# Performance work log

Hardware: AMD Instinct MI355X
Metric: run time of the kernel (lower is better)

Reference implementation:

```python
import jax, jax.numpy as jnp
import numpy as np

B, R, N, DN, DR, H, Q, NB = 32, 10, 512, 128, 128, 128, 256, 16


def setup_inputs() -> dict:
    key = jax.random.key(0)
    ks = jax.random.split(key, 14)
    inp = {
        'node_features': jax.random.normal(ks[0], (B, N, DN), jnp.float32),
        'relation_features': jax.random.normal(ks[1], (B, R, DR), jnp.float32),
        'adj': jax.random.uniform(ks[2], (B, R, N, N), jnp.float32),
        'obs': jax.random.normal(ks[3], (B, Q, H), jnp.float32),
        'node_mask': jnp.ones((B, N), jnp.float32),
        'obs_mask': jnp.ones((B, Q), jnp.float32),
        # RGCN params (single layer: hidden_dims=[128])
        'Wb': jax.random.normal(ks[4], (NB, (DN + DR) * R), jnp.float32) * 0.02,  # bottleneck (no bias)
        'Ww': jax.random.normal(ks[5], (H, NB), jnp.float32) * 0.1,               # weight (no bias)
        'rgcn_bias': jnp.zeros((), jnp.float32),                                   # scalar bias (filled 0)
        # ContextQueryAttention params
        'w_C': jax.random.normal(ks[6], (H,), jnp.float32) * 0.05,
        'w_Q': jax.random.normal(ks[7], (H,), jnp.float32) * 0.05,
        'w_CQ': jax.random.normal(ks[8], (H,), jnp.float32) * 0.05,
        'cq_bias': jnp.zeros((), jnp.float32),
        # ReprAggregator output linear (shared for both directions)
        'lin_W': jax.random.normal(ks[9], (H, 4 * H), jnp.float32) * 0.02,
        'lin_b': jnp.zeros((H,), jnp.float32),
    }
    return inp


def _masked_softmax(s, mask, axis):
    return jax.nn.softmax(jnp.where(mask > 0, s, -jnp.inf), axis=axis)


def _rgcn(node_features, relation_features, adj, Wb, Ww, rgcn_bias):
    b, n = node_features.shape[0], node_features.shape[1]
    # per-relation concat: (B,R,N,DN+DR)
    nf = jnp.broadcast_to(node_features[:, None], (b, R, n, node_features.shape[-1]))
    rf = jnp.broadcast_to(relation_features[:, :, None, :], (b, R, n, relation_features.shape[-1]))
    cat = jnp.concatenate([nf, rf], axis=-1)
    # per-relation bmm, gathered in relation order along feature dim: (B,N,R*(DN+DR))
    sup = jnp.einsum('brnm,brmd->bnrd', adj, cat)
    sup = sup.reshape(b, n, R * cat.shape[-1])
    h = sup @ Wb.T            # (B,N,NB)
    h = h @ Ww.T              # (B,N,H)
    return jax.nn.sigmoid(h + rgcn_bias)


def _cqattn(ctx, query, ctx_mask, query_mask, w_C, w_Q, w_CQ, cq_bias):
    # trilinear similarity: (B,Lc,Lq)
    res_C = ctx @ w_C                                  # (B,Lc)
    res_Q = query @ w_Q                                # (B,Lq)
    res_CQ = jnp.einsum('bch,bqh->bcq', ctx * w_CQ, query)
    S = res_C[:, :, None] + res_Q[:, None, :] + res_CQ + cq_bias
    s_ctx = _masked_softmax(S, ctx_mask[:, :, None], axis=1)     # softmax over ctx dim
    s_query = _masked_softmax(S, query_mask[:, None, :], axis=2)  # softmax over query dim
    P = jnp.einsum('bcq,bqh->bch', s_query, query)
    Qm = jnp.einsum('bcq,bdq,bdh->bch', s_query, s_ctx, ctx)
    return jnp.concatenate([ctx, P, ctx * P, ctx * Qm], axis=-1)  # (B,Lc,4H)


def reference(node_features, relation_features, adj, obs, node_mask, obs_mask,
              Wb, Ww, rgcn_bias, w_C, w_Q, w_CQ, cq_bias, lin_W, lin_b):
    # GraphEncoder (single RGCN layer)
    node_repr = _rgcn(node_features, relation_features, adj, Wb, Ww, rgcn_bias)
    # ReprAggregator between obs text repr and node repr
    a1 = _cqattn(obs, node_repr, obs_mask, node_mask, w_C, w_Q, w_CQ, cq_bias)
    a2 = _cqattn(node_repr, obs, node_mask, obs_mask, w_C, w_Q, w_CQ, cq_bias)
    h_og = a1 @ lin_W.T + lin_b   # (B,Q,H)
    h_go = a2 @ lin_W.T + lin_b   # (B,N,H)
    return h_og, h_go
```

## Files before the change

kernel.cpp:

```cpp
#include <hip/hip_runtime.h>
#include <hip/hip_bf16.h>
#include <stdint.h>

typedef unsigned short u16;
typedef __attribute__((ext_vector_type(8))) short short8;
typedef __attribute__((ext_vector_type(4))) float f32x4;

#define DEVI static __device__ __forceinline__

constexpr int B = 32, R = 10, N = 512, H = 128, Q = 256, NB = 16;
constexpr int KWB = 2560;

DEVI u16 f2u(float f) { return __builtin_bit_cast(unsigned short, __float2bfloat16(f)); }
DEVI float u2f(u16 u) { union { uint32_t i; float f; } c; c.i = ((uint32_t)u) << 16; return c.f; }

DEVI float wredmax(float v) { for (int o = 32; o; o >>= 1) v = fmaxf(v, __shfl_xor(v, o)); return v; }
DEVI float wredsum(float v) { for (int o = 32; o; o >>= 1) v += __shfl_xor(v, o); return v; }

DEVI short8 cvt8(const float* p) {
  float4 f0 = *(const float4*)p;
  float4 f1 = *(const float4*)(p + 4);
  short8 v;
  v[0] = (short)f2u(f0.x); v[1] = (short)f2u(f0.y);
  v[2] = (short)f2u(f0.z); v[3] = (short)f2u(f0.w);
  v[4] = (short)f2u(f1.x); v[5] = (short)f2u(f1.y);
  v[6] = (short)f2u(f1.z); v[7] = (short)f2u(f1.w);
  return v;
}

__global__ __launch_bounds__(256) void k_prep(
    const float* __restrict__ linW, u16* __restrict__ linWb,
    const float* __restrict__ Wb, u16* __restrict__ WbB,
    const float* __restrict__ Ww, u16* __restrict__ WwB,
    const float* __restrict__ rf, float* __restrict__ vv,
    const float* __restrict__ obs, const float* __restrict__ wC,
    const float* __restrict__ wQ, const float* __restrict__ wCQ,
    u16* __restrict__ obsW, float* __restrict__ a_o, float* __restrict__ d_o,
    u16* __restrict__ obsT) {
  int bid = blockIdx.x, t = threadIdx.x;
  __shared__ float sa[4], sd[4];
  __shared__ u16 tile[32][33];
  if (bid < 64) {
    int i = bid * 256 + t;
    float4 f = ((const float4*)linW)[i];
    ushort4 o;
    o.x = f2u(f.x); o.y = f2u(f.y); o.z = f2u(f.z); o.w = f2u(f.w);
    ((ushort4*)linWb)[i] = o;
  } else if (bid < 144) {
    int rk = (bid - 64) * 2 + (t >> 7);
    int d = t & 127;
    int r = rk / NB, k = rk % NB;
    WbB[(long)rk * 128 + d] = f2u(Wb[(long)k * KWB + r * 256 + d]);
  } else if (bid < 160) {
    int idx = (bid - 144) * 256 + t;
    int h = idx >> 5, kb = idx & 31;
    WwB[idx] = (kb < NB) ? f2u(Ww[h * NB + kb]) : (u16)0;
  } else if (bid < 1440) {
    int w = t >> 6, lane = t & 63;
    int gid = (bid - 160) * 4 + w;
    int b = gid / (R * NB), rk = gid % (R * NB), r = rk / NB, k = rk % NB;
    float s = 0.f;
    for (int dd = 0; dd < 2; ++dd) {
      int d = lane + dd * 64;
      s += rf[((long)b * R + r) * H + d] * Wb[(long)k * KWB + r * 256 + 128 + d];
    }
    s = wredsum(s);
    if (lane == 0) vv[((long)b * R + r) * NB + k] = s;
  } else if (bid < 5536) {
    int row = (bid - 1440) * 2 + (t >> 7);
    int tt = t & 127;
    float x = obs[(long)row * H + tt];
    obsW[(long)row * H + tt] = f2u(x * wCQ[tt]);
    float aa = wredsum(x * wC[tt]);
    float dd2 = wredsum(x * wQ[tt]);
    int wv = t >> 6;
    if ((t & 63) == 0) { sa[wv] = aa; sd[wv] = dd2; }
    __syncthreads();
    if ((t & 127) == 0) {
      int h = t >> 7;
      a_o[row] = sa[h * 2] + sa[h * 2 + 1];
      d_o[row] = sd[h * 2] + sd[h * 2 + 1];
    }
  } else {
    int id = bid - 5536;
    int cx = id & 3, ry = (id >> 2) & 7, b = id >> 5;
    int c0 = cx * 32, r0 = ry * 32;
    int tx = t & 31, ty = t >> 5;
    for (int i = 0; i < 4; i++) {
      int r = r0 + ty + i * 8, c = c0 + tx;
      tile[ty + i * 8][tx] = f2u(obs[((long)b * Q + r) * H + c]);
    }
    __syncthreads();
    for (int i = 0; i < 4; i++) {
      int c = c0 + ty + i * 8, r = r0 + tx;
      obsT[((long)b * H + c) * Q + r] = tile[tx][ty + i * 8];
    }
  }
}

template <bool AF32, bool BF32, int CMODE, bool TRANSC, int BMODE, bool RGRID, int UNROLL>
__global__ __launch_bounds__(64) void gemm_bt(const void* __restrict__ Av, const void* __restrict__ Btv,
                                              void* __restrict__ Cp, float* __restrict__ C2,
                                              const float* __restrict__ bias,
                                              int Mdim, int Ndim, int Kdim,
                                              long sA, long sBt, long sC, long sC2) {
  int batch = blockIdx.y;
  int ab = batch, bb = batch;
  if (RGRID) { ab = batch % R; bb = batch / R; }
  int ntn = Ndim >> 4;
  int mt = blockIdx.x / ntn, nt = blockIdx.x % ntn;
  int lane = threadIdx.x;
  int rw = lane & 15, kq = lane >> 4;
  long aoff = (long)ab * sA + (long)(mt * 16 + rw) * Kdim + kq * 8;
  long boff = (long)bb * sBt + (long)(nt * 16 + rw) * Kdim + kq * 8;
  f32x4 acc = {0.f, 0.f, 0.f, 0.f};
#pragma unroll UNROLL
  for (int k = 0; k < Kdim; k += 32) {
    short8 av, bv;
    if (AF32) av = cvt8((const float*)Av + aoff + k);
    else      av = *(const short8*)((const u16*)Av + aoff + k);
    if (BF32) bv = cvt8((const float*)Btv + boff + k);
    else      bv = *(const short8*)((const u16*)Btv + boff + k);
    acc = __builtin_amdgcn_mfma_f32_16x16x32_bf16(av, bv, acc, 0, 0, 0);
  }
  int gc = nt * 16 + rw;
  float cb = (BMODE == 1) ? bias[gc] : 0.f;
  for (int i = 0; i < 4; i++) {
    int gr = mt * 16 + (kq * 4 + i);
    float val = acc[i] + cb;
    if (BMODE == 2) val += bias[(long)batch * NB + gr];
    if (CMODE == 2) {
      ((float*)Cp)[(long)batch * sC + (long)gr * Ndim + gc] = val;
      C2[(long)batch * sC2 + (long)gc * Mdim + gr] = val;
    } else {
      long idx = TRANSC ? ((long)gc * Mdim + gr) : ((long)gr * Ndim + gc);
      if (CMODE == 1) ((float*)Cp)[(long)batch * sC + idx] = val;
      else            ((u16*)Cp)[(long)batch * sC + idx] = f2u(val);
    }
  }
}

__global__ __launch_bounds__(256) void k_rgcn(
    const float* __restrict__ adj, const u16* __restrict__ tT,
    const u16* __restrict__ WwB, const float* __restrict__ rb,
    const float* __restrict__ wC, const float* __restrict__ wQ,
    u16* __restrict__ nr, u16* __restrict__ nrT,
    float* __restrict__ b_n, float* __restrict__ c_n) {
  int ntile = blockIdx.x, b = blockIdx.y;
  int n0 = ntile * 16;
  int tid = threadIdx.x;
  int w = tid >> 6, lane = tid & 63;
  int rw = lane & 15, kq = lane >> 4;
  __shared__ float hred[4][16][17];
  __shared__ __align__(16) u16 hbf[16][32];
  __shared__ float bpc[4][16][2];
  float rbv = rb[0];

  f32x4 acc = {0.f, 0.f, 0.f, 0.f};
#pragma unroll 4
  for (int j = 0; j < 40; ++j) {
    int kkk = w + 4 * j;
    int r = kkk >> 4, k = (kkk & 15) * 32;
    short8 av = cvt8(adj + (((long)(b * R + r) * N) + n0 + rw) * N + k + kq * 8);
    short8 bv = *(const short8*)(tT + ((long)(b * R + r) * NB + rw) * N + k + kq * 8);
    acc = __builtin_amdgcn_mfma_f32_16x16x32_bf16(av, bv, acc, 0, 0, 0);
  }
  for (int i = 0; i < 4; i++) hred[w][kq * 4 + i][rw] = acc[i];
  __syncthreads();
  {
    int n = tid >> 4, kb = tid & 15;
    float s = hred[0][n][kb] + hred[1][n][kb] + hred[2][n][kb] + hred[3][n][kb];
    hbf[n][kb] = f2u(s);
    hbf[n][kb + 16] = 0;
  }
  __syncthreads();

  float bsum[4] = {0.f, 0.f, 0.f, 0.f}, csum[4] = {0.f, 0.f, 0.f, 0.f};
  for (int half = 0; half < 2; ++half) {
    int nt = w * 2 + half;
    short8 av = *(const short8*)&hbf[rw][kq * 8];
    short8 bv = *(const short8*)(WwB + (long)(nt * 16 + rw) * 32 + kq * 8);
    f32x4 a2 = {0.f, 0.f, 0.f, 0.f};
    a2 = __builtin_amdgcn_mfma_f32_16x16x32_bf16(av, bv, a2, 0, 0, 0);
    int h = nt * 16 + rw;
    float wq = wQ[h], wc = wC[h];
    for (int i = 0; i < 4; i++) {
      float s = 1.f / (1.f + expf(-(a2[i] + rbv)));
      int n = n0 + kq * 4 + i;
      u16 sv = f2u(s);
      nr[((long)b * N + n) * H + h] = sv;
      nrT[((long)b * H + h) * N + n] = sv;
      bsum[i] += s * wq;
      csum[i] += s * wc;
    }
  }
  for (int i = 0; i < 4; i++) {
    for (int o = 8; o; o >>= 1) { bsum[i] += __shfl_xor(bsum[i], o); csum[i] += __shfl_xor(csum[i], o); }
  }
  if (rw == 0)
    for (int i = 0; i < 4; i++) { bpc[w][kq * 4 + i][0] = bsum[i]; bpc[w][kq * 4 + i][1] = csum[i]; }
  __syncthreads();
  if (tid < 32) {
    int ns = tid & 15, which = tid >> 4;
    float s = bpc[0][ns][which] + bpc[1][ns][which] + bpc[2][ns][which] + bpc[3][ns][which];
    (which ? c_n : b_n)[(long)b * N + n0 + ns] = s;
  }
}

__global__ __launch_bounds__(64) void k_mm(const u16* __restrict__ obsW, const u16* __restrict__ nr,
                                           u16* __restrict__ S, u16* __restrict__ ST) {
  int bx = blockIdx.x;
  int mt = bx >> 2, ng = bx & 3;
  int b = blockIdx.y;
  int lane = threadIdx.x;
  int rw = lane & 15, kq = lane >> 4;
  const u16* ap = obsW + ((long)b * Q + mt * 16 + rw) * H + kq * 8;
  const u16* bp = nr + ((long)b * N + ng * 128 + rw) * H + kq * 8;
  f32x4 acc[8] = {};
  for (int k = 0; k < H; k += 32) {
    short8 av = *(const short8*)(ap + k);
#pragma unroll
    for (int nt = 0; nt < 8; nt++) {
      short8 bv = *(const short8*)(bp + (long)nt * 16 * H + k);
      acc[nt] = __builtin_amdgcn_mfma_f32_16x16x32_bf16(av, bv, acc[nt], 0, 0, 0);
    }
  }
#pragma unroll
  for (int nt = 0; nt < 8; nt++) {
    int gc = ng * 128 + nt * 16 + rw;
    for (int i = 0; i < 4; i++) {
      int gr = mt * 16 + kq * 4 + i;
      u16 v = f2u(acc[nt][i]);
      S[((long)b * Q + gr) * N + gc] = v;
      ST[((long)b * N + gc) * Q + gr] = v;
    }
  }
}

__global__ __launch_bounds__(256) void k_soft_both(
    const u16* __restrict__ S, const u16* __restrict__ ST,
    const float* __restrict__ b_n, const float* __restrict__ c_n,
    const float* __restrict__ a_o, const float* __restrict__ d_o,
    const float* __restrict__ nmask, const float* __restrict__ omask,
    u16* __restrict__ sq1, u16* __restrict__ sc2,
    u16* __restrict__ sc1T, u16* __restrict__ sq2) {
  int bid = blockIdx.x;
  __shared__ float s1a[4], s2a[4];
  if (bid < B * Q) {
    int b = bid / Q;
    int t = threadIdx.x;
    long ro = bid;
    float v1[2], v2[2];
    for (int i = 0; i < 2; i++) {
      int n = t + 256 * i;
      float mv = u2f(S[ro * N + n]);
      bool on = nmask[(long)b * N + n] > 0.f;
      v1[i] = on ? b_n[(long)b * N + n] + mv : -1e30f;
      v2[i] = on ? c_n[(long)b * N + n] + mv : -1e30f;
    }
    float m1 = wredmax(fmaxf(v1[0], v1[1]));
    float m2 = wredmax(fmaxf(v2[0], v2[1]));
    int wv = t >> 6;
    if ((t & 63) == 0) { s1a[wv] = m1; s2a[wv] = m2; }
    __syncthreads();
    m1 = fmaxf(fmaxf(s1a[0], s1a[1]), fmaxf(s1a[2], s1a[3]));
    m2 = fmaxf(fmaxf(s2a[0], s2a[1]), fmaxf(s2a[2], s2a[3]));
    __syncthreads();
    float e1[2], e2[2];
    e1[0] = expf(v1[0] - m1); e1[1] = expf(v1[1] - m1);
    e2[0] = expf(v2[0] - m2); e2[1] = expf(v2[1] - m2);
    float s1 = wredsum(e1[0] + e1[1]);
    float s2 = wredsum(e2[0] + e2[1]);
    if ((t & 63) == 0) { s1a[wv] = s1; s2a[wv] = s2; }
    __syncthreads();
    float r1 = 1.f / (s1a[0] + s1a[1] + s1a[2] + s1a[3]);
    float r2 = 1.f / (s2a[0] + s2a[1] + s2a[2] + s2a[3]);
    for (int i = 0; i < 2; i++) {
      int n = t + 256 * i;
      sq1[ro * N + n] = f2u(e1[i] * r1);
      sc2[ro * N + n] = f2u(e2[i] * r2);
    }
  } else {
    int id = bid - B * Q;
    int b = id / N;
    int o = threadIdx.x;
    long rn = id;
    float mv = u2f(ST[rn * Q + o]);
    bool on = omask[(long)b * Q + o] > 0.f;
    float v1 = on ? a_o[(long)b * Q + o] + mv : -1e30f;
    float v2 = on ? d_o[(long)b * Q + o] + mv : -1e30f;
    float m1 = wredmax(v1), m2 = wredmax(v2);
    int wv = o >> 6;
    if ((o & 63) == 0) { s1a[wv] = m1; s2a[wv] = m2; }
    __syncthreads();
    m1 = fmaxf(fmaxf(s1a[0], s1a[1]), fmaxf(s1a[2], s1a[3]));
    m2 = fmaxf(fmaxf(s2a[0], s2a[1]), fmaxf(s2a[2], s2a[3]));
    __syncthreads();
    float e1 = expf(v1 - m1), e2 = expf(v2 - m2);
    float s1 = wredsum(e1), s2 = wredsum(e2);
    if ((o & 63) == 0) { s1a[wv] = s1; s2a[wv] = s2; }
    __syncthreads();
    float r1 = 1.f / (s1a[0] + s1a[1] + s1a[2] + s1a[3]);
    float r2 = 1.f / (s2a[0] + s2a[1] + s2a[2] + s2a[3]);
    sc1T[rn * Q + o] = f2u(e1 * r1);
    sq2[rn * Q + o] = f2u(e2 * r2);
  }
}

struct GPar {
  const u16* A; const u16* Bt; u16* C;
  int Mdim; int Kdim; long sA, sBt, sC; int tc;
};
__global__ __launch_bounds__(64) void gemm_quad8(GPar p0, GPar p1, GPar p2, GPar p3) {
  int z = blockIdx.z;
  GPar p = (z == 0) ? p0 : (z == 1) ? p1 : (z == 2) ? p2 : p3;
  int mt = blockIdx.x;
  if (mt * 16 >= p.Mdim) return;
  int batch = blockIdx.y;
  int lane = threadIdx.x;
  int rw = lane & 15, kq = lane >> 4;
  const u16* ap = p.A + (long)batch * p.sA + (long)(mt * 16 + rw) * p.Kdim + kq * 8;
  const u16* bp = p.Bt + (long)batch * p.sBt + (long)rw * p.Kdim + kq * 8;
  f32x4 acc[8] = {};
  for (int k = 0; k < p.Kdim; k += 32) {
    short8 av = *(const short8*)(ap + k);
#pragma unroll
    for (int nt = 0; nt < 8; nt++) {
      short8 bv = *(const short8*)(bp + (long)nt * 16 * p.Kdim + k);
      acc[nt] = __builtin_amdgcn_mfma_f32_16x16x32_bf16(av, bv, acc[nt], 0, 0, 0);
    }
  }
#pragma unroll
  for (int nt = 0; nt < 8; nt++) {
    int gc = nt * 16 + rw;
    for (int i = 0; i < 4; i++) {
      int gr = mt * 16 + kq * 4 + i;
      long idx = p.tc ? ((long)gc * p.Mdim + gr) : ((long)gr * H + gc);
      p.C[(long)batch * p.sC + idx] = f2u(acc[nt][i]);
    }
  }
}

__global__ __launch_bounds__(64) void gemm_cat2(
    const float* __restrict__ obs, const u16* __restrict__ nrr,
    const u16* __restrict__ P1, const u16* __restrict__ Qm1,
    const u16* __restrict__ P2, const u16* __restrict__ Qm2,
    const u16* __restrict__ Wt, const float* __restrict__ bias,
    float* __restrict__ out0, float* __restrict__ out1) {
  int z = blockIdx.z;
  int Mdim = z ? N : Q;
  int mt = blockIdx.x;
  if (mt * 16 >= Mdim) return;
  int batch = blockIdx.y;
  const u16* P = z ? P2 : P1;
  const u16* Qm = z ? Qm2 : Qm1;
  float* out = z ? out1 : out0;
  int lane = threadIdx.x;
  int rw = lane & 15, kq = lane >> 4;
  long arow = (long)batch * Mdim + mt * 16 + rw;
  const u16* bp = Wt + (long)rw * (4 * H) + kq * 8;
  f32x4 acc[8] = {};
  for (int k = 0; k < 4 * H; k += 32) {
    int sec = k >> 7;
    int off = (k & 127) + kq * 8;
    long rb2 = arow * H + off;
    short8 av;
    if (sec == 0) {
      if (!z) av = cvt8(obs + rb2);
      else    av = *(const short8*)(nrr + rb2);
    } else if (sec == 1) {
      av = *(const short8*)(P + rb2);
    } else {
      float xf[8];
      if (!z) {
        const float* xp = obs + rb2;
        float4 f0 = *(const float4*)xp;
        float4 f1 = *(const float4*)(xp + 4);
        xf[0] = f0.x; xf[1] = f0.y; xf[2] = f0.z; xf[3] = f0.w;
        xf[4] = f1.x; xf[5] = f1.y; xf[6] = f1.z; xf[7] = f1.w;
      } else {
        short8 xv = *(const short8*)(nrr + rb2);
        for (int i = 0; i < 8; i++) xf[i] = u2f((u16)xv[i]);
      }
      short8 pv = *(const short8*)((sec == 2 ? P : Qm) + rb2);
      for (int i = 0; i < 8; i++) av[i] = (short)f2u(xf[i] * u2f((u16)pv[i]));
    }
#pragma unroll
    for (int nt = 0; nt < 8; nt++) {
      short8 bv = *(const short8*)(bp + (long)nt * 16 * (4 * H) + k);
      acc[nt] = __builtin_amdgcn_mfma_f32_16x16x32_bf16(av, bv, acc[nt], 0, 0, 0);
    }
  }
#pragma unroll
  for (int nt = 0; nt < 8; nt++) {
    int gc = nt * 16 + rw;
    float cb = bias[gc];
    for (int i = 0; i < 4; i++) {
      int gr = mt * 16 + kq * 4 + i;
      out[((long)batch * Mdim + gr) * H + gc] = acc[nt][i] + cb;
    }
  }
}

extern "C" void kernel_launch(void* const* d_in, const int* in_sizes, int n_in,
                              void* d_out, int out_size, void* d_ws, size_t ws_size,
                              hipStream_t stream) {
  const float* nf    = (const float*)d_in[0];
  const float* rf    = (const float*)d_in[1];
  const float* adj   = (const float*)d_in[2];
  const float* obs   = (const float*)d_in[3];
  const float* nmask = (const float*)d_in[4];
  const float* omask = (const float*)d_in[5];
  const float* Wb    = (const float*)d_in[6];
  const float* Ww    = (const float*)d_in[7];
  const float* rb    = (const float*)d_in[8];
  const float* wC    = (const float*)d_in[9];
  const float* wQ    = (const float*)d_in[10];
  const float* wCQ   = (const float*)d_in[11];
  const float* linW  = (const float*)d_in[13];
  const float* linb  = (const float*)d_in[14];
  float* outp = (float*)d_out;

  char* w = (char*)d_ws;
  auto alloc = [&](size_t bytes) { char* p = w; w += (bytes + 255) & ~(size_t)255; return p; };
  u16*   linWb = (u16*)  alloc((size_t)H * 4 * H * 2);
  u16*   WbB   = (u16*)  alloc((size_t)R * NB * 128 * 2);
  u16*   WwB   = (u16*)  alloc((size_t)H * 32 * 2);
  float* vv    = (float*)alloc((size_t)B * R * NB * 4);
  u16*   obsW  = (u16*)  alloc((size_t)B * Q * H * 2);
  u16*   obsT  = (u16*)  alloc((size_t)B * H * Q * 2);
  float* a_o   = (float*)alloc((size_t)B * Q * 4);
  float* d_o   = (float*)alloc((size_t)B * Q * 4);
  float* b_n   = (float*)alloc((size_t)B * N * 4);
  float* c_n   = (float*)alloc((size_t)B * N * 4);
  u16*   nr    = (u16*)  alloc((size_t)B * N * H * 2);
  u16*   nrT   = (u16*)  alloc((size_t)B * H * N * 2);
  u16*   tT    = (u16*)  alloc((size_t)B * R * NB * N * 2);
  u16*   S     = (u16*)  alloc((size_t)B * Q * N * 2);
  u16*   ST    = (u16*)  alloc((size_t)B * N * Q * 2);
  u16*   sq1   = (u16*)  alloc((size_t)B * Q * N * 2);
  u16*   sc2   = (u16*)  alloc((size_t)B * Q * N * 2);
  u16*   sc1T  = (u16*)  alloc((size_t)B * N * Q * 2);
  u16*   sq2   = (u16*)  alloc((size_t)B * N * Q * 2);
  u16*   P1    = (u16*)  alloc((size_t)B * Q * H * 2);
  u16*   T1T   = (u16*)  alloc((size_t)B * H * N * 2);
  u16*   Qm1   = (u16*)  alloc((size_t)B * Q * H * 2);
  u16*   P2    = (u16*)  alloc((size_t)B * N * H * 2);
  u16*   T2T   = (u16*)  alloc((size_t)B * H * Q * 2);
  u16*   Qm2   = (u16*)  alloc((size_t)B * N * H * 2);

  k_prep<<<6560, 256, 0, stream>>>(linW, linWb, Wb, WbB, Ww, WwB,
                                   rf, vv, obs, wC, wQ, wCQ, obsW, a_o, d_o, obsT);
  gemm_bt<false, true, 0, false, 2, true, 2><<<dim3(N / 16, B * R), 64, 0, stream>>>(
      WbB, nf, tT, nullptr, vv, NB, N, H, (long)NB * 128, (long)N * H, (long)NB * N, 0);
  k_rgcn<<<dim3(N / 16, B), 256, 0, stream>>>(adj, tT, WwB, rb, wC, wQ, nr, nrT, b_n, c_n);
  k_mm<<<dim3((Q / 16) * (N / 128), B), 64, 0, stream>>>(obsW, nr, S, ST);
  k_soft_both<<<B * Q + B * N, 256, 0, stream>>>(S, ST, b_n, c_n, a_o, d_o, nmask, omask,
                                                 sq1, sc2, sc1T, sq2);
  GPar pP1  = {sq1,  nrT,  P1,  Q, N, (long)Q * N, (long)H * N, (long)Q * H, 0};
  GPar pT2T = {sc2,  nrT,  T2T, Q, N, (long)Q * N, (long)H * N, (long)H * Q, 1};
  GPar pT1T = {sc1T, obsT, T1T, N, Q, (long)N * Q, (long)H * Q, (long)H * N, 1};
  GPar pP2  = {sq2,  obsT, P2,  N, Q, (long)N * Q, (long)H * Q, (long)N * H, 0};
  gemm_quad8<<<dim3(N / 16, B, 4), 64, 0, stream>>>(pP1, pT2T, pT1T, pP2);
  GPar pQm1 = {sq1, T1T, Qm1, Q, N, (long)Q * N, (long)H * N, (long)Q * H, 0};
  GPar pQm2 = {sq2, T2T, Qm2, N, Q, (long)N * Q, (long)H * Q, (long)N * H, 0};
  gemm_quad8<<<dim3(N / 16, B, 2), 64, 0, stream>>>(pQm1, pQm2, pQm1, pQm2);
  gemm_cat2<<<dim3(N / 16, B, 2), 64, 0, stream>>>(obs, nr, P1, Qm1, P2, Qm2,
                                                   linWb, linb, outp, outp + (long)B * Q * H);

  (void)in_sizes; (void)n_in; (void)out_size; (void)ws_size;
}
```

Baseline: 297.6 us.

## Fuse score GEMM with row softmax and restructure RGCN projection kernels

Replaces the generic per-relation projection GEMM with a kernel that stages the node-feature tile in swizzled LDS once and reuses it across all relations. The RGCN kernel now uses 512 threads so the adjacency reduction is split across 8 waves. The score GEMM is fused with the row-wise (over nodes) softmax, which drops the S buffer and one pass over it; only the transposed scores are still written for the column softmax, which runs as its own kernel. This trades fewer launches and less global traffic for larger blocks and extra cross-wave reductions in LDS.

```diff
diff --git a/kernel.cpp b/kernel.cpp
--- a/kernel.cpp
+++ b/kernel.cpp
@@ -98,49 +98,47 @@
   }
 }
 
-template <bool AF32, bool BF32, int CMODE, bool TRANSC, int BMODE, bool RGRID, int UNROLL>
-__global__ __launch_bounds__(64) void gemm_bt(const void* __restrict__ Av, const void* __restrict__ Btv,
-                                              void* __restrict__ Cp, float* __restrict__ C2,
-                                              const float* __restrict__ bias,
-                                              int Mdim, int Ndim, int Kdim,
-                                              long sA, long sBt, long sC, long sC2) {
-  int batch = blockIdx.y;
-  int ab = batch, bb = batch;
-  if (RGRID) { ab = batch % R; bb = batch / R; }
-  int ntn = Ndim >> 4;
-  int mt = blockIdx.x / ntn, nt = blockIdx.x % ntn;
-  int lane = threadIdx.x;
+__global__ __launch_bounds__(512) void k_tt(const u16* __restrict__ WbB, const float* __restrict__ nf,
+                                            const float* __restrict__ vv, u16* __restrict__ tT) {
+  int bx = blockIdx.x, b = blockIdx.y;
+  int t = threadIdx.x;
+  __shared__ __align__(16) u16 tile[128][128];
+  {
+    int row = t >> 2, q = (t & 3) * 32;
+    const float* src = nf + ((long)b * N + bx * 128 + row) * H + q;
+    int sw = (row & 7) << 3;
+    for (int j = 0; j < 4; j++) {
+      short8 v = cvt8(src + j * 8);
+      *(short8*)&tile[row][(q + j * 8) ^ sw] = v;
+    }
+  }
+  __syncthreads();
+  int w = t >> 6, lane = t & 63;
   int rw = lane & 15, kq = lane >> 4;
-  long aoff = (long)ab * sA + (long)(mt * 16 + rw) * Kdim + kq * 8;
-  long boff = (long)bb * sBt + (long)(nt * 16 + rw) * Kdim + kq * 8;
-  f32x4 acc = {0.f, 0.f, 0.f, 0.f};
-#pragma unroll UNROLL
-  for (int k = 0; k < Kdim; k += 32) {
-    short8 av, bv;
-    if (AF32) av = cvt8((const float*)Av + aoff + k);
-    else      av = *(const short8*)((const u16*)Av + aoff + k);
-    if (BF32) bv = cvt8((const float*)Btv + boff + k);
-    else      bv = *(const short8*)((const u16*)Btv + boff + k);
-    acc = __builtin_amdgcn_mfma_f32_16x16x32_bf16(av, bv, acc, 0, 0, 0);
-  }
-  int gc = nt * 16 + rw;
-  float cb = (BMODE == 1) ? bias[gc] : 0.f;
-  for (int i = 0; i < 4; i++) {
-    int gr = mt * 16 + (kq * 4 + i);
-    float val = acc[i] + cb;
-    if (BMODE == 2) val += bias[(long)batch * NB + gr];
-    if (CMODE == 2) {
-      ((float*)Cp)[(long)batch * sC + (long)gr * Ndim + gc] = val;
-      C2[(long)batch * sC2 + (long)gc * Mdim + gr] = val;
-    } else {
-      long idx = TRANSC ? ((long)gc * Mdim + gr) : ((long)gr * Ndim + gc);
-      if (CMODE == 1) ((float*)Cp)[(long)batch * sC + idx] = val;
-      else            ((u16*)Cp)[(long)batch * sC + idx] = f2u(val);
-    }
-  }
-}
-
-__global__ __launch_bounds__(256) void k_rgcn(
+  for (int r = w; r < R; r += 8) {
+    f32x4 acc[8] = {};
+    for (int kit = 0; kit < H; kit += 32) {
+      short8 av = *(const short8*)(WbB + ((long)r * NB + rw) * 128 + kit + kq * 8);
+#pragma unroll
+      for (int nt = 0; nt < 8; nt++) {
+        int brow = nt * 16 + rw;
+        short8 bv = *(const short8*)&tile[brow][(kit + kq * 8) ^ ((brow & 7) << 3)];
+        acc[nt] = __builtin_amdgcn_mfma_f32_16x16x32_bf16(av, bv, acc[nt], 0, 0, 0);
+      }
+    }
+    long rbase = (long)(b * R + r) * NB;
+#pragma unroll
+    for (int nt = 0; nt < 8; nt++) {
+      int gc = bx * 128 + nt * 16 + rw;
+      for (int i = 0; i < 4; i++) {
+        int gr = kq * 4 + i;
+        tT[(rbase + gr) * N + gc] = f2u(acc[nt][i] + vv[rbase + gr]);
+      }
+    }
+  }
+}
+
+__global__ __launch_bounds__(512) void k_rgcn(
     const float* __restrict__ adj, const u16* __restrict__ tT,
     const u16* __restrict__ WwB, const float* __restrict__ rb,
     const float* __restrict__ wC, const float* __restrict__ wQ,
@@ -151,15 +149,15 @@
   int tid = threadIdx.x;
   int w = tid >> 6, lane = tid & 63;
   int rw = lane & 15, kq = lane >> 4;
-  __shared__ float hred[4][16][17];
+  __shared__ float hred[8][16][17];
   __shared__ __align__(16) u16 hbf[16][32];
-  __shared__ float bpc[4][16][2];
+  __shared__ float bpc[8][16][2];
   float rbv = rb[0];
 
   f32x4 acc = {0.f, 0.f, 0.f, 0.f};
 #pragma unroll 4
-  for (int j = 0; j < 40; ++j) {
-    int kkk = w + 4 * j;
+  for (int j = 0; j < 20; ++j) {
+    int kkk = w + 8 * j;
     int r = kkk >> 4, k = (kkk & 15) * 32;
     short8 av = cvt8(adj + (((long)(b * R + r) * N) + n0 + rw) * N + k + kq * 8);
     short8 bv = *(const short8*)(tT + ((long)(b * R + r) * NB + rw) * N + k + kq * 8);
@@ -167,32 +165,30 @@
   }
   for (int i = 0; i < 4; i++) hred[w][kq * 4 + i][rw] = acc[i];
   __syncthreads();
-  {
+  if (tid < 256) {
     int n = tid >> 4, kb = tid & 15;
-    float s = hred[0][n][kb] + hred[1][n][kb] + hred[2][n][kb] + hred[3][n][kb];
+    float s = 0.f;
+    for (int ww = 0; ww < 8; ww++) s += hred[ww][n][kb];
     hbf[n][kb] = f2u(s);
     hbf[n][kb + 16] = 0;
   }
   __syncthreads();
 
-  float bsum[4] = {0.f, 0.f, 0.f, 0.f}, csum[4] = {0.f, 0.f, 0.f, 0.f};
-  for (int half = 0; half < 2; ++half) {
-    int nt = w * 2 + half;
-    short8 av = *(const short8*)&hbf[rw][kq * 8];
-    short8 bv = *(const short8*)(WwB + (long)(nt * 16 + rw) * 32 + kq * 8);
-    f32x4 a2 = {0.f, 0.f, 0.f, 0.f};
-    a2 = __builtin_amdgcn_mfma_f32_16x16x32_bf16(av, bv, a2, 0, 0, 0);
-    int h = nt * 16 + rw;
-    float wq = wQ[h], wc = wC[h];
-    for (int i = 0; i < 4; i++) {
-      float s = 1.f / (1.f + expf(-(a2[i] + rbv)));
-      int n = n0 + kq * 4 + i;
-      u16 sv = f2u(s);
-      nr[((long)b * N + n) * H + h] = sv;
-      nrT[((long)b * H + h) * N + n] = sv;
-      bsum[i] += s * wq;
-      csum[i] += s * wc;
-    }
+  short8 av = *(const short8*)&hbf[rw][kq * 8];
+  short8 bv = *(const short8*)(WwB + (long)(w * 16 + rw) * 32 + kq * 8);
+  f32x4 a2 = {0.f, 0.f, 0.f, 0.f};
+  a2 = __builtin_amdgcn_mfma_f32_16x16x32_bf16(av, bv, a2, 0, 0, 0);
+  int h = w * 16 + rw;
+  float wq = wQ[h], wc = wC[h];
+  float bsum[4], csum[4];
+  for (int i = 0; i < 4; i++) {
+    float s = 1.f / (1.f + expf(-(a2[i] + rbv)));
+    int n = n0 + kq * 4 + i;
+    u16 sv = f2u(s);
+    nr[((long)b * N + n) * H + h] = sv;
+    nrT[((long)b * H + h) * N + n] = sv;
+    bsum[i] = s * wq;
+    csum[i] = s * wc;
   }
   for (int i = 0; i < 4; i++) {
     for (int o = 8; o; o >>= 1) { bsum[i] += __shfl_xor(bsum[i], o); csum[i] += __shfl_xor(csum[i], o); }
@@ -202,109 +198,126 @@
   __syncthreads();
   if (tid < 32) {
     int ns = tid & 15, which = tid >> 4;
-    float s = bpc[0][ns][which] + bpc[1][ns][which] + bpc[2][ns][which] + bpc[3][ns][which];
+    float s = 0.f;
+    for (int ww = 0; ww < 8; ww++) s += bpc[ww][ns][which];
     (which ? c_n : b_n)[(long)b * N + n0 + ns] = s;
   }
 }
 
-__global__ __launch_bounds__(64) void k_mm(const u16* __restrict__ obsW, const u16* __restrict__ nr,
-                                           u16* __restrict__ S, u16* __restrict__ ST) {
-  int bx = blockIdx.x;
-  int mt = bx >> 2, ng = bx & 3;
-  int b = blockIdx.y;
-  int lane = threadIdx.x;
+__global__ __launch_bounds__(512) void k_mm_soft(
+    const u16* __restrict__ obsW, const u16* __restrict__ nr,
+    const float* __restrict__ b_n, const float* __restrict__ c_n,
+    const float* __restrict__ nmask,
+    u16* __restrict__ sq1, u16* __restrict__ sc2, u16* __restrict__ ST) {
+  int mt = blockIdx.x, b = blockIdx.y;
+  int tid = threadIdx.x;
+  int w = tid >> 6, lane = tid & 63;
   int rw = lane & 15, kq = lane >> 4;
+  __shared__ float sm1[8][16], sm2[8][16], ss1[8][16], ss2[8][16];
+
   const u16* ap = obsW + ((long)b * Q + mt * 16 + rw) * H + kq * 8;
-  const u16* bp = nr + ((long)b * N + ng * 128 + rw) * H + kq * 8;
-  f32x4 acc[8] = {};
+  const u16* bp = nr + ((long)b * N + w * 64 + rw) * H + kq * 8;
+  f32x4 acc[4] = {};
   for (int k = 0; k < H; k += 32) {
     short8 av = *(const short8*)(ap + k);
 #pragma unroll
-    for (int nt = 0; nt < 8; nt++) {
+    for (int nt = 0; nt < 4; nt++) {
       short8 bv = *(const short8*)(bp + (long)nt * 16 * H + k);
       acc[nt] = __builtin_amdgcn_mfma_f32_16x16x32_bf16(av, bv, acc[nt], 0, 0, 0);
     }
   }
-#pragma unroll
-  for (int nt = 0; nt < 8; nt++) {
-    int gc = ng * 128 + nt * 16 + rw;
-    for (int i = 0; i < 4; i++) {
-      int gr = mt * 16 + kq * 4 + i;
-      u16 v = f2u(acc[nt][i]);
-      S[((long)b * Q + gr) * N + gc] = v;
-      ST[((long)b * N + gc) * Q + gr] = v;
-    }
-  }
-}
-
-__global__ __launch_bounds__(256) void k_soft_both(
-    const u16* __restrict__ S, const u16* __restrict__ ST,
-    const float* __restrict__ b_n, const float* __restrict__ c_n,
-    const float* __restrict__ a_o, const float* __restrict__ d_o,
-    const float* __restrict__ nmask, const float* __restrict__ omask,
-    u16* __restrict__ sq1, u16* __restrict__ sc2,
-    u16* __restrict__ sc1T, u16* __restrict__ sq2) {
-  int bid = blockIdx.x;
+  float bn[4], cn[4];
+  bool mk[4];
+  int gcv[4];
+#pragma unroll
+  for (int nt = 0; nt < 4; nt++) {
+    int gc = w * 64 + nt * 16 + rw;
+    gcv[nt] = gc;
+    mk[nt] = nmask[(long)b * N + gc] > 0.f;
+    bn[nt] = b_n[(long)b * N + gc];
+    cn[nt] = c_n[(long)b * N + gc];
+  }
+#pragma unroll
+  for (int nt = 0; nt < 4; nt++) {
+    long stb = ((long)b * N + gcv[nt]) * Q + mt * 16 + kq * 4;
+    for (int i = 0; i < 4; i++) ST[stb + i] = f2u(acc[nt][i]);
+  }
+  float m1[4], m2[4];
+  for (int i = 0; i < 4; i++) { m1[i] = -1e30f; m2[i] = -1e30f; }
+#pragma unroll
+  for (int nt = 0; nt < 4; nt++)
+    for (int i = 0; i < 4; i++) {
+      float s = acc[nt][i];
+      if (mk[nt]) { m1[i] = fmaxf(m1[i], s + bn[nt]); m2[i] = fmaxf(m2[i], s + cn[nt]); }
+    }
+  for (int i = 0; i < 4; i++)
+    for (int o = 8; o; o >>= 1) { m1[i] = fmaxf(m1[i], __shfl_xor(m1[i], o)); m2[i] = fmaxf(m2[i], __shfl_xor(m2[i], o)); }
+  if (rw == 0)
+    for (int i = 0; i < 4; i++) { sm1[w][kq * 4 + i] = m1[i]; sm2[w][kq * 4 + i] = m2[i]; }
+  __syncthreads();
+  for (int i = 0; i < 4; i++) {
+    float g1 = -1e30f, g2 = -1e30f;
+    for (int ww = 0; ww < 8; ww++) { g1 = fmaxf(g1, sm1[ww][kq * 4 + i]); g2 = fmaxf(g2, sm2[ww][kq * 4 + i]); }
+    m1[i] = g1; m2[i] = g2;
+  }
+  float e1[4][4], e2[4][4];
+  float s1[4] = {0.f, 0.f, 0.f, 0.f}, s2[4] = {0.f, 0.f, 0.f, 0.f};
+#pragma unroll
+  for (int nt = 0; nt < 4; nt++)
+    for (int i = 0; i < 4; i++) {
+      float s = acc[nt][i];
+      float a = mk[nt] ? expf(s + bn[nt] - m1[i]) : 0.f;
+      float c = mk[nt] ? expf(s + cn[nt] - m2[i]) : 0.f;
+      e1[nt][i] = a; e2[nt][i] = c;
+      s1[i] += a; s2[i] += c;
+    }
+  for (int i = 0; i < 4; i++)
+    for (int o = 8; o; o >>= 1) { s1[i] += __shfl_xor(s1[i], o); s2[i] += __shfl_xor(s2[i], o); }
+  if (rw == 0)
+    for (int i = 0; i < 4; i++) { ss1[w][kq * 4 + i] = s1[i]; ss2[w][kq * 4 + i] = s2[i]; }
+  __syncthreads();
+  float r1[4], r2[4];
+  for (int i = 0; i < 4; i++) {
+    float g1 = 0.f, g2 = 0.f;
+    for (int ww = 0; ww < 8; ww++) { g1 += ss1[ww][kq * 4 + i]; g2 += ss2[ww][kq * 4 + i]; }
+    r1[i] = 1.f / g1; r2[i] = 1.f / g2;
+  }
+#pragma unroll
+  for (int nt = 0; nt < 4; nt++)
+    for (int i = 0; i < 4; i++) {
+      long ob = ((long)b * Q + mt * 16 + kq * 4 + i) * N + gcv[nt];
+      sq1[ob] = f2u(e1[nt][i] * r1[i]);
+      sc2[ob] = f2u(e2[nt][i] * r2[i]);
+    }
+}
+
+__global__ __launch_bounds__(256) void k_soft_col(
+    const u16* __restrict__ ST, const float* __restrict__ a_o, const float* __restrict__ d_o,
+    const float* __restrict__ omask, u16* __restrict__ sc1T, u16* __restrict__ sq2) {
+  int id = blockIdx.x;
+  int b = id / N;
+  int o = threadIdx.x;
+  long rn = id;
   __shared__ float s1a[4], s2a[4];
-  if (bid < B * Q) {
-    int b = bid / Q;
-    int t = threadIdx.x;
-    long ro = bid;
-    float v1[2], v2[2];
-    for (int i = 0; i < 2; i++) {
-      int n = t + 256 * i;
-      float mv = u2f(S[ro * N + n]);
-      bool on = nmask[(long)b * N + n] > 0.f;
-      v1[i] = on ? b_n[(long)b * N + n] + mv : -1e30f;
-      v2[i] = on ? c_n[(long)b * N + n] + mv : -1e30f;
-    }
-    float m1 = wredmax(fmaxf(v1[0], v1[1]));
-    float m2 = wredmax(fmaxf(v2[0], v2[1]));
-    int wv = t >> 6;
-    if ((t & 63) == 0) { s1a[wv] = m1; s2a[wv] = m2; }
-    __syncthreads();
-    m1 = fmaxf(fmaxf(s1a[0], s1a[1]), fmaxf(s1a[2], s1a[3]));
-    m2 = fmaxf(fmaxf(s2a[0], s2a[1]), fmaxf(s2a[2], s2a[3]));
-    __syncthreads();
-    float e1[2], e2[2];
-    e1[0] = expf(v1[0] - m1); e1[1] = expf(v1[1] - m1);
-    e2[0] = expf(v2[0] - m2); e2[1] = expf(v2[1] - m2);
-    float s1 = wredsum(e1[0] + e1[1]);
-    float s2 = wredsum(e2[0] + e2[1]);
-    if ((t & 63) == 0) { s1a[wv] = s1; s2a[wv] = s2; }
-    __syncthreads();
-    float r1 = 1.f / (s1a[0] + s1a[1] + s1a[2] + s1a[3]);
-    float r2 = 1.f / (s2a[0] + s2a[1] + s2a[2] + s2a[3]);
-    for (int i = 0; i < 2; i++) {
-      int n = t + 256 * i;
-      sq1[ro * N + n] = f2u(e1[i] * r1);
-      sc2[ro * N + n] = f2u(e2[i] * r2);
-    }
-  } else {
-    int id = bid - B * Q;
-    int b = id / N;
-    int o = threadIdx.x;
-    long rn = id;
-    float mv = u2f(ST[rn * Q + o]);
-    bool on = omask[(long)b * Q + o] > 0.f;
-    float v1 = on ? a_o[(long)b * Q + o] + mv : -1e30f;
-    float v2 = on ? d_o[(long)b * Q + o] + mv : -1e30f;
-    float m1 = wredmax(v1), m2 = wredmax(v2);
-    int wv = o >> 6;
-    if ((o & 63) == 0) { s1a[wv] = m1; s2a[wv] = m2; }
-    __syncthreads();
-    m1 = fmaxf(fmaxf(s1a[0], s1a[1]), fmaxf(s1a[2], s1a[3]));
-    m2 = fmaxf(fmaxf(s2a[0], s2a[1]), fmaxf(s2a[2], s2a[3]));
-    __syncthreads();
-    float e1 = expf(v1 - m1), e2 = expf(v2 - m2);
-    float s1 = wredsum(e1), s2 = wredsum(e2);
-    if ((o & 63) == 0) { s1a[wv] = s1; s2a[wv] = s2; }
-    __syncthreads();
-    float r1 = 1.f / (s1a[0] + s1a[1] + s1a[2] + s1a[3]);
-    float r2 = 1.f / (s2a[0] + s2a[1] + s2a[2] + s2a[3]);
-    sc1T[rn * Q + o] = f2u(e1 * r1);
-    sq2[rn * Q + o] = f2u(e2 * r2);
-  }
+  float mv = u2f(ST[rn * Q + o]);
+  bool on = omask[(long)b * Q + o] > 0.f;
+  float v1 = on ? a_o[(long)b * Q + o] + mv : -1e30f;
+  float v2 = on ? d_o[(long)b * Q + o] + mv : -1e30f;
+  float m1 = wredmax(v1), m2 = wredmax(v2);
+  int wv = o >> 6;
+  if ((o & 63) == 0) { s1a[wv] = m1; s2a[wv] = m2; }
+  __syncthreads();
+  m1 = fmaxf(fmaxf(s1a[0], s1a[1]), fmaxf(s1a[2], s1a[3]));
+  m2 = fmaxf(fmaxf(s2a[0], s2a[1]), fmaxf(s2a[2], s2a[3]));
+  __syncthreads();
+  float e1 = expf(v1 - m1), e2 = expf(v2 - m2);
+  float s1 = wredsum(e1), s2 = wredsum(e2);
+  if ((o & 63) == 0) { s1a[wv] = s1; s2a[wv] = s2; }
+  __syncthreads();
+  float r1 = 1.f / (s1a[0] + s1a[1] + s1a[2] + s1a[3]);
+  float r2 = 1.f / (s2a[0] + s2a[1] + s2a[2] + s2a[3]);
+  sc1T[rn * Q + o] = f2u(e1 * r1);
+  sq2[rn * Q + o] = f2u(e2 * r2);
 }
 
 struct GPar {
@@ -436,7 +449,6 @@
   u16*   nr    = (u16*)  alloc((size_t)B * N * H * 2);
   u16*   nrT   = (u16*)  alloc((size_t)B * H * N * 2);
   u16*   tT    = (u16*)  alloc((size_t)B * R * NB * N * 2);
-  u16*   S     = (u16*)  alloc((size_t)B * Q * N * 2);
   u16*   ST    = (u16*)  alloc((size_t)B * N * Q * 2);
   u16*   sq1   = (u16*)  alloc((size_t)B * Q * N * 2);
   u16*   sc2   = (u16*)  alloc((size_t)B * Q * N * 2);
@@ -451,12 +463,10 @@
 
   k_prep<<<6560, 256, 0, stream>>>(linW, linWb, Wb, WbB, Ww, WwB,
                                    rf, vv, obs, wC, wQ, wCQ, obsW, a_o, d_o, obsT);
-  gemm_bt<false, true, 0, false, 2, true, 2><<<dim3(N / 16, B * R), 64, 0, stream>>>(
-      WbB, nf, tT, nullptr, vv, NB, N, H, (long)NB * 128, (long)N * H, (long)NB * N, 0);
-  k_rgcn<<<dim3(N / 16, B), 256, 0, stream>>>(adj, tT, WwB, rb, wC, wQ, nr, nrT, b_n, c_n);
-  k_mm<<<dim3((Q / 16) * (N / 128), B), 64, 0, stream>>>(obsW, nr, S, ST);
-  k_soft_both<<<B * Q + B * N, 256, 0, stream>>>(S, ST, b_n, c_n, a_o, d_o, nmask, omask,
-                                                 sq1, sc2, sc1T, sq2);
+  k_tt<<<dim3(N / 128, B), 512, 0, stream>>>(WbB, nf, vv, tT);
+  k_rgcn<<<dim3(N / 16, B), 512, 0, stream>>>(adj, tT, WwB, rb, wC, wQ, nr, nrT, b_n, c_n);
+  k_mm_soft<<<dim3(Q / 16, B), 512, 0, stream>>>(obsW, nr, b_n, c_n, nmask, sq1, sc2, ST);
+  k_soft_col<<<B * N, 256, 0, stream>>>(ST, a_o, d_o, omask, sc1T, sq2);
   GPar pP1  = {sq1,  nrT,  P1,  Q, N, (long)Q * N, (long)H * N, (long)Q * H, 0};
   GPar pT2T = {sc2,  nrT,  T2T, Q, N, (long)Q * N, (long)H * N, (long)H * Q, 1};
   GPar pT1T = {sc1T, obsT, T1T, N, Q, (long)N * Q, (long)H * Q, (long)H * N, 1};
```

Result: faster. 282.4 us (-5.1%).
